# Kernel tuning notes

Measured on AMD Instinct MI355X. Metric: run time of the kernel, lower is better.

## Reference

```python
import jax, jax.numpy as jnp
import numpy as np

N_GRAPHS = 512  # number of graphs in the batch
S2S_STEPS = 3   # Set2Set processing_steps


def segment_softmax(e, seg, num_seg):
    m = jax.ops.segment_max(e, seg, num_segments=num_seg)
    ex = jnp.exp(e - m[seg])
    s = jax.ops.segment_sum(ex, seg, num_segments=num_seg)
    return ex / s[seg]


def setup_inputs() -> dict:
    key = jax.random.key(0)
    ks = jax.random.split(key, 24)
    N, E, Fin, Fe, D = 30000, 480000, 25, 14, 256
    s = 0.05
    inp = {
        "x": jax.random.normal(ks[0], (N, Fin), jnp.float32),
        "edge_attr": jax.random.normal(ks[1], (E, Fe), jnp.float32),
        # lin0
        "W0": jax.random.normal(ks[2], (Fin, D), jnp.float32) * s,
        "b0": jnp.zeros((D,), jnp.float32),
        # DMPNN edge-message MLP: [x_src || e_attr] -> D -> D
        "Wm1": jax.random.normal(ks[3], (D + Fe, D), jnp.float32) * s,
        "bm1": jnp.zeros((D,), jnp.float32),
        "Wm2": jax.random.normal(ks[4], (D, D), jnp.float32) * s,
        "bm2": jnp.zeros((D,), jnp.float32),
        # node (root) update
        "Wr": jax.random.normal(ks[5], (D, D), jnp.float32) * s,
        "br": jnp.zeros((D,), jnp.float32),
        # Set2Set LSTM: input 2D -> hidden D
        "Wih": jax.random.normal(ks[6], (2 * D, 4 * D), jnp.float32) * s,
        "Whh": jax.random.normal(ks[7], (D, 4 * D), jnp.float32) * s,
        "bl": jnp.zeros((4 * D,), jnp.float32),
        # readout MLP
        "W1": jax.random.normal(ks[8], (2 * D, D), jnp.float32) * s,
        "b1": jnp.zeros((D,), jnp.float32),
        "W2": jax.random.normal(ks[9], (D, 1), jnp.float32) * s,
        "b2": jnp.zeros((1,), jnp.float32),
        "edge_index": jax.random.randint(ks[10], (2, E), 0, N, jnp.int32),
        "batch": jnp.sort(jax.random.randint(ks[11], (N,), 0, N_GRAPHS, jnp.int32)),
    }
    return inp


def reference(x, edge_attr, W0, b0, Wm1, bm1, Wm2, bm2, Wr, br,
              Wih, Whh, bl, W1, b1, W2, b2, edge_index, batch):
    N = x.shape[0]
    # lin0 + relu
    h0 = jax.nn.relu(x @ W0 + b0)  # [N, D]
    # DMPNNLayer2: edge-conditioned message, sum-aggregate, root update (eval: no dropout)
    src, dst = edge_index[0], edge_index[1]
    m = jax.nn.relu(jnp.concatenate([h0[src], edge_attr], axis=-1) @ Wm1 + bm1)  # [E, D]
    m = m @ Wm2 + bm2
    agg = jax.ops.segment_sum(m, dst, num_segments=N)  # [N, D]
    out = jax.nn.relu(h0 @ Wr + br + agg)  # relu in top-level forward, massage_depth=1
    # Set2Set pooling (processing_steps=3)
    D = out.shape[1]
    B = N_GRAPHS
    q_star = jnp.zeros((B, 2 * D), out.dtype)
    h = jnp.zeros((B, D), out.dtype)
    c = jnp.zeros((B, D), out.dtype)
    for _ in range(S2S_STEPS):
        gates = q_star @ Wih + h @ Whh + bl  # [B, 4D]
        i, f, g, o = jnp.split(gates, 4, axis=-1)
        c = jax.nn.sigmoid(f) * c + jax.nn.sigmoid(i) * jnp.tanh(g)
        h = jax.nn.sigmoid(o) * jnp.tanh(c)
        e = jnp.sum(out * h[batch], axis=-1)              # [N]
        a = segment_softmax(e, batch, B)                  # [N]
        r = jax.ops.segment_sum(a[:, None] * out, batch, num_segments=B)  # [B, D]
        q_star = jnp.concatenate([h, r], axis=-1)
    # readout (eval: dropout identity)
    y = jax.nn.relu(q_star @ W1 + b1)
    y = y @ W2 + b2
    return y.reshape(-1)
```

## Files before the change

### kernel.cpp

```cpp
#include <hip/hip_runtime.h>

typedef unsigned short u16;
typedef unsigned char u8;
typedef unsigned int u32;
using s16x8 = __attribute__((ext_vector_type(8))) short;
using s16x4 = __attribute__((ext_vector_type(4))) short;
using f32x4 = __attribute__((ext_vector_type(4))) float;

#define DEV static __device__ __forceinline__

DEV float b2f(u16 u) { return __uint_as_float(((u32)u) << 16); }
DEV u16 f2bu(float f) {
    u32 u = __float_as_uint(f);
    u32 r = (u + 0x7FFFu + ((u >> 16) & 1u)) >> 16;
    return (u16)r;
}
DEV float sigm(float x) { return 1.0f / (1.0f + expf(-x)); }

DEV float ldv(const void* p, int i, int f32flag) {
    if (f32flag) return ((const float*)p)[i];
    return b2f(((const u16*)p)[i]);
}
DEV void stv(void* p, int i, float v, int f32flag) {
    if (f32flag) ((float*)p)[i] = v;
    else ((u16*)p)[i] = f2bu(v);
}

DEV int lower_bound(const int* b, int n, int v) {
    int lo = 0, hi = n;
    while (lo < hi) { int mid = (lo + hi) >> 1; if (b[mid] < v) lo = mid + 1; else hi = mid; }
    return lo;
}

__global__ void DMPNN_Change_678604832935_kernel(int* p) {
    if (p && threadIdx.x == 0 && blockIdx.x == 0) p[0] = 1;
}

__global__ void detect_kernel(const void* x, int* flag) {
    __shared__ int cnt[128];
    int tid = threadIdx.x;
    if (tid < 128) {
        u16 v = ((const u16*)x)[tid];
        int e = (v >> 7) & 0xFF;
        cnt[tid] = (e >= 100 && e <= 141) ? 1 : 0;
    }
    __syncthreads();
    if (tid == 0) {
        int s = 0;
        for (int i = 0; i < 128; ++i) s += cnt[i];
        flag[0] = (s < 110) ? 1 : 0;
    }
}

__global__ void fillv_kernel(void* out, const int* flag, float v) {
    int i = blockIdx.x * 256 + threadIdx.x;
    if (i < 512) stv(out, i, v, flag[0]);
}

__global__ void zero_kernel(float* p, int n) {
    int i = blockIdx.x * 256 + threadIdx.x;
    int stride = gridDim.x * 256;
    for (; i < n; i += stride) p[i] = 0.0f;
}

__global__ void zero2_kernel(float* a, int na, float* b, int nb) {
    int i = blockIdx.x * 256 + threadIdx.x;
    int stride = gridDim.x * 256;
    for (int j = i; j < na; j += stride) a[j] = 0.0f;
    for (int j = i; j < nb; j += stride) b[j] = 0.0f;
}

__global__ void hist_kernel(const int* __restrict__ eidx, u32* __restrict__ cnt) {
    int i = blockIdx.x * 256 + threadIdx.x;
    if (i < 480000) atomicAdd(&cnt[eidx[480000 + i]], 1u);
}

__global__ void scan1_kernel(const u32* __restrict__ cnt, u32* __restrict__ part) {
    __shared__ u32 s[256];
    int i = blockIdx.x * 256 + threadIdx.x;
    s[threadIdx.x] = (i < 30000) ? cnt[i] : 0u;
    __syncthreads();
    for (int st = 128; st > 0; st >>= 1) {
        if (threadIdx.x < st) s[threadIdx.x] += s[threadIdx.x + st];
        __syncthreads();
    }
    if (threadIdx.x == 0) part[blockIdx.x] = s[0];
}

__global__ void scan2_kernel(const u32* __restrict__ part, u32* __restrict__ pexcl, int nb) {
    int tid = threadIdx.x;
    u32 v = (tid < nb) ? part[tid] : 0u;
    u32 x = v;
    #pragma unroll
    for (int off = 1; off < 64; off <<= 1) {
        u32 t = __shfl_up(x, off, 64);
        if ((tid & 63) >= off) x += t;
    }
    __shared__ u32 wsum;
    if (tid == 63) wsum = x;
    __syncthreads();
    u32 add = (tid >= 64) ? wsum : 0u;
    if (tid < nb) pexcl[tid] = x + add - v;
}

__global__ void scan3_kernel(u32* __restrict__ cursor, const u32* __restrict__ pexcl) {
    __shared__ u32 s[256];
    int b = blockIdx.x, tid = threadIdx.x;
    int i = b * 256 + tid;
    u32 v = (i < 30000) ? cursor[i] : 0u;
    s[tid] = v;
    __syncthreads();
    for (int off = 1; off < 256; off <<= 1) {
        u32 t = (tid >= off) ? s[tid - off] : 0u;
        __syncthreads();
        s[tid] += t;
        __syncthreads();
    }
    u32 excl = s[tid] - v + pexcl[b];
    if (i < 30000) cursor[i] = excl;
}

__global__ void scatter_kernel(const int* __restrict__ eidx, u32* __restrict__ cursor,
                               u16* __restrict__ permLo, u8* __restrict__ permHi,
                               u16* __restrict__ srcW) {
    int i = blockIdx.x * 256 + threadIdx.x;
    if (i < 480000) {
        int d = eidx[480000 + i];
        u32 pos = atomicAdd(&cursor[d], 1u);
        permLo[pos] = (u16)(i & 0xFFFF);
        permHi[pos] = (u8)(i >> 16);
        if (srcW) srcW[pos] = (u16)eidx[i];
    }
}

__global__ void to_blocked_all(const void* Wm1, const void* Wm2, const void* Wr,
                               const void* Wih, const void* Whh, const int* flag,
                               u16* Wm1b, u16* Wm2b, u16* Wrb, u16* Wcatb) {
    const int T1 = 9 * 4 * 256 * 8;
    const int T2 = T1 + 8 * 4 * 256 * 8;
    const int T3 = T2 + 8 * 4 * 256 * 8;
    const int T4 = T3 + 24 * 4 * 1024 * 8;
    int idx = blockIdx.x * 256 + threadIdx.x;
    if (idx >= T4) return;
    int f32 = flag[0];
    if (idx < T3) {
        const void* src; u16* dst; int K; int l;
        if (idx < T1)      { src = Wm1; dst = Wm1b; K = 270; l = idx; }
        else if (idx < T2) { src = Wm2; dst = Wm2b; K = 256; l = idx - T1; }
        else               { src = Wr;  dst = Wrb;  K = 256; l = idx - T2; }
        int c = l & 7;
        int n = (l >> 3) & 255;
        int jk = l >> 11;
        int j = jk & 3, kt = jk >> 2;
        int k = kt * 32 + j * 8 + c;
        u16 v = 0;
        if (k < K) v = f2bu(ldv(src, k * 256 + n, f32));
        dst[l] = v;
    } else {
        int l = idx - T3;
        int c = l & 7;
        int n = (l >> 3) & 1023;
        int jk = l >> 13;
        int j = jk & 3, kt = jk >> 2;
        int k = kt * 32 + j * 8 + c;
        u16 v = 0;
        if (k < 512) v = f2bu(ldv(Wih, k * 1024 + n, f32));
        else if (k < 768) v = f2bu(ldv(Whh, (k - 512) * 1024 + n, f32));
        Wcatb[l] = v;
    }
}

__global__ __launch_bounds__(256) void lin0_kernel(const void* x, const void* W0,
                                                   const void* b0, const int* flag,
                                                   u16* h0b) {
    int f32 = flag[0];
    int n0 = blockIdx.x * 8, tid = threadIdx.x;
    __shared__ float xs[8][26];
    if (tid < 200) {
        int nn = tid / 25, k = tid % 25;
        xs[nn][k] = ldv(x, (n0 + nn) * 25 + k, f32);
    }
    __syncthreads();
    float wr[25];
    #pragma unroll
    for (int k = 0; k < 25; ++k) wr[k] = ldv(W0, k * 256 + tid, f32);
    float bias = ldv(b0, tid, f32);
    #pragma unroll
    for (int nn = 0; nn < 8; ++nn) {
        float a = bias;
        #pragma unroll
        for (int k = 0; k < 25; ++k) a += xs[nn][k] * wr[k];
        h0b[(n0 + nn) * 256 + tid] = f2bu(fmaxf(a, 0.0f));
    }
}

__global__ __launch_bounds__(256) void lin0q_kernel(
    const void* x, const void* W0, const void* b0, const int* flag,
    const u16* __restrict__ Wm1b, u16* __restrict__ h0b, u16* __restrict__ Qb) {
    __shared__ __attribute__((aligned(16))) u16 As[64 * 264];
    __shared__ float xs[64][26];
    const int f32 = flag[0];
    const int tid = threadIdx.x;
    const int w = tid >> 6, lane = tid & 63, quad = lane >> 4, mrow = lane & 15;
    const int row0 = blockIdx.x * 64;
    const int colb = w * 64 + mrow;

    for (int idx = tid; idx < 64 * 25; idx += 256) {
        int i = idx / 25, k = idx - i * 25;
        int row = row0 + i;
        xs[i][k] = (row < 30000) ? ldv(x, row * 25 + k, f32) : 0.0f;
    }
    float wr[25];
    #pragma unroll
    for (int k = 0; k < 25; ++k) wr[k] = ldv(W0, k * 256 + tid, f32);
    float bias = ldv(b0, tid, f32);
    __syncthreads();
    for (int i = 0; i < 64; ++i) {
        float a = bias;
        #pragma unroll
        for (int k = 0; k < 25; ++k) a += xs[i][k] * wr[k];
        u16 hb = f2bu(fmaxf(a, 0.0f));
        As[i * 264 + tid] = hb;
        int row = row0 + i;
        if (row < 30000) h0b[row * 256 + tid] = hb;
    }
    __syncthreads();

    f32x4 acc[4][4];
    f32x4 fzero = {0.f, 0.f, 0.f, 0.f};
    #pragma unroll
    for (int mi = 0; mi < 4; ++mi)
        #pragma unroll
        for (int ni = 0; ni < 4; ++ni) acc[mi][ni] = fzero;

    for (int kt = 0; kt < 8; ++kt) {
        s16x8 af[4], bf[4];
        #pragma unroll
        for (int ni = 0; ni < 4; ++ni)
            bf[ni] = *(const s16x8*)(Wm1b + (((kt * 4 + quad) * 256) + colb + ni * 16) * 8);
        #pragma unroll
        for (int mi = 0; mi < 4; ++mi)
            af[mi] = *(const s16x8*)(As + (mi * 16 + mrow) * 264 + kt * 32 + quad * 8);
        #pragma unroll
        for (int mi = 0; mi < 4; ++mi)
            #pragma unroll
            for (int ni = 0; ni < 4; ++ni)
                acc[mi][ni] = __builtin_amdgcn_mfma_f32_16x16x32_bf16(af[mi], bf[ni], acc[mi][ni], 0, 0, 0);
    }

    #pragma unroll
    for (int mi = 0; mi < 4; ++mi)
        #pragma unroll
        for (int rg = 0; rg < 4; ++rg) {
            int row = row0 + mi * 16 + quad * 4 + rg;
            if (row >= 30000) continue;
            #pragma unroll
            for (int ni = 0; ni < 4; ++ni)
                Qb[row * 256 + colb + ni * 16] = f2bu(acc[mi][ni][rg]);
        }
}

__global__ __launch_bounds__(256) void qgen_kernel(
    const u16* __restrict__ h0b, const u16* __restrict__ Wm1b,
    u16* __restrict__ Qb) {
    __shared__ __attribute__((aligned(16))) u16 As[64 * 264];
    const int tid = threadIdx.x;
    const int w = tid >> 6, lane = tid & 63, quad = lane >> 4, mrow = lane & 15;
    const int row0 = blockIdx.x * 64;
    const int colb = w * 64 + mrow;
    const int r = tid >> 2, sub = tid & 3;

    {
        int row = row0 + r;
        u16* arow = As + r * 264;
        #pragma unroll
        for (int j = 0; j < 8; ++j) {
            int c0 = sub * 64 + j * 8;
            s16x8 v = {0, 0, 0, 0, 0, 0, 0, 0};
            if (row < 30000) v = *(const s16x8*)(h0b + row * 256 + c0);
            *(s16x8*)(arow + c0) = v;
        }
    }
    __syncthreads();

    f32x4 acc[4][4];
    f32x4 fzero = {0.f, 0.f, 0.f, 0.f};
    #pragma unroll
    for (int mi = 0; mi < 4; ++mi)
        #pragma unroll
        for (int ni = 0; ni < 4; ++ni) acc[mi][ni] = fzero;

    for (int kt = 0; kt < 8; ++kt) {
        s16x8 af[4], bf[4];
        #pragma unroll
        for (int ni = 0; ni < 4; ++ni)
            bf[ni] = *(const s16x8*)(Wm1b + (((kt * 4 + quad) * 256) + colb + ni * 16) * 8);
        #pragma unroll
        for (int mi = 0; mi < 4; ++mi)
            af[mi] = *(const s16x8*)(As + (mi * 16 + mrow) * 264 + kt * 32 + quad * 8);
        #pragma unroll
        for (int mi = 0; mi < 4; ++mi)
            #pragma unroll
            for (int ni = 0; ni < 4; ++ni)
                acc[mi][ni] = __builtin_amdgcn_mfma_f32_16x16x32_bf16(af[mi], bf[ni], acc[mi][ni], 0, 0, 0);
    }

    #pragma unroll
    for (int mi = 0; mi < 4; ++mi)
        #pragma unroll
        for (int rg = 0; rg < 4; ++rg) {
            int row = row0 + mi * 16 + quad * 4 + rg;
            if (row >= 30000) continue;
            #pragma unroll
            for (int ni = 0; ni < 4; ++ni)
                Qb[row * 256 + colb + ni * 16] = f2bu(acc[mi][ni][rg]);
        }
}

#define MAXD 96
__global__ __launch_bounds__(256) void edge_mfma_node2_kernel(
    const u16* __restrict__ Qb, const void* __restrict__ eattr,
    const u16* __restrict__ srcW,
    const u16* __restrict__ permLo, const u8* __restrict__ permHi,
    const u32* __restrict__ cursor,
    const u16* __restrict__ Wm1b, const void* __restrict__ bm1,
    const int* __restrict__ flag, u16* __restrict__ aggB) {
    const int f32 = flag[0];
    const int n = blockIdx.x, tid = threadIdx.x;
    const int w = tid >> 6, lane = tid & 63, quad = lane >> 4, mrow = lane & 15;
    const int beg = (n > 0) ? (int)cursor[n - 1] : 0;
    const int end = (int)cursor[n];
    __shared__ int eids[MAXD];
    __shared__ int srcl[MAXD];
    __shared__ int sorted_s[MAXD];
    __shared__ int sortedSrc[MAXD];
    __shared__ __attribute__((aligned(16))) u16 Ae[16 * 40];

    const int colb = w * 64 + mrow;
    s16x8 bf[4];
    float bm1c[4];
    #pragma unroll
    for (int ni = 0; ni < 4; ++ni) {
        bf[ni] = *(const s16x8*)(Wm1b + (((32 + quad) * 256) + colb + ni * 16) * 8);
        bm1c[ni] = ldv(bm1, colb + ni * 16, f32);
    }

    float psum[4] = {0.f, 0.f, 0.f, 0.f};
    const f32x4 fzero = {0.f, 0.f, 0.f, 0.f};

    for (int base = beg; base < end; base += MAXD) {
        int wcnt = end - base; if (wcnt > MAXD) wcnt = MAXD;
        if (tid < wcnt) {
            int si = base + tid;
            eids[tid] = (int)permLo[si] | ((int)permHi[si] << 16);
            srcl[tid] = (int)srcW[si];
        }
        __syncthreads();
        if (tid < wcnt) {
            int key = eids[tid], r2 = 0;
            for (int j = 0; j < wcnt; ++j) r2 += (eids[j] < key);
            sorted_s[r2] = key;
            sortedSrc[r2] = srcl[tid];
        }
        __syncthreads();

        for (int cb = 0; cb < wcnt; cb += 16) {
            {
                int row = tid >> 4, c = tid & 15;
                int gi = cb + row;
                int e = (gi < wcnt) ? sorted_s[gi] : -1;
                u16 v = 0;
                if (e >= 0 && c < 14) v = f2bu(ldv(eattr, e * 14 + c, f32));
                Ae[row * 40 + c] = v;
                Ae[row * 40 + 16 + c] = 0;
            }
            __syncthreads();

            float qv[4][4];
            #pragma unroll
            for (int rg = 0; rg < 4; ++rg) {
                int gi = cb + quad * 4 + rg;
                int sidx = (gi < wcnt) ? sortedSrc[gi] : 0;
                const u16* qrow = Qb + sidx * 256;
                #pragma unroll
                for (int ni = 0; ni < 4; ++ni)
                    qv[rg][ni] = b2f(qrow[colb + ni * 16]);
            }

            s16x8 af = *(const s16x8*)(Ae + mrow * 40 + quad * 8);
            f32x4 acc[4];
            #pragma unroll
            for (int ni = 0; ni < 4; ++ni)
                acc[ni] = __builtin_amdgcn_mfma_f32_16x16x32_bf16(af, bf[ni], fzero, 0, 0, 0);

            #pragma unroll
            for (int rg = 0; rg < 4; ++rg) {
                if (cb + quad * 4 + rg < wcnt) {
                    #pragma unroll
                    for (int ni = 0; ni < 4; ++ni)
                        psum[ni] += fmaxf(acc[ni][rg] + bm1c[ni] + qv[rg][ni], 0.0f);
                }
            }
            __syncthreads();
        }
    }

    #pragma unroll
    for (int ni = 0; ni < 4; ++ni) {
        float v = psum[ni];
        v += __shfl_xor(v, 16, 64);
        v += __shfl_xor(v, 32, 64);
        psum[ni] = v;
    }
    if (quad == 0) {
        #pragma unroll
        for (int ni = 0; ni < 4; ++ni)
            aggB[n * 256 + colb + ni * 16] = f2bu(psum[ni]);
    }
}

__global__ __launch_bounds__(256) void edge_mfma_node_kernel(
    const u16* __restrict__ Qb, const void* __restrict__ eattr,
    const int* __restrict__ eidx,
    const u16* __restrict__ permLo, const u8* __restrict__ permHi,
    const u32* __restrict__ cursor,
    const u16* __restrict__ Wm1b, const void* __restrict__ bm1,
    const int* __restrict__ flag, float* __restrict__ aggP) {
    const int f32 = flag[0];
    const int n = blockIdx.x, tid = threadIdx.x;
    const int w = tid >> 6, lane = tid & 63, quad = lane >> 4, mrow = lane & 15;
    const int beg = (n > 0) ? (int)cursor[n - 1] : 0;
    const int end = (int)cursor[n];
    __shared__ int eids[MAXD];
    __shared__ int sorted_s[MAXD];
    __shared__ int srcs16[16];
    __shared__ __attribute__((aligned(16))) u16 Ae[16 * 40];

    const int colb = w * 64 + mrow;
    s16x8 bf[4];
    float bm1c[4];
    #pragma unroll
    for (int ni = 0; ni < 4; ++ni) {
        bf[ni] = *(const s16x8*)(Wm1b + (((32 + quad) * 256) + colb + ni * 16) * 8);
        bm1c[ni] = ldv(bm1, colb + ni * 16, f32);
    }

    float psum[4] = {0.f, 0.f, 0.f, 0.f};
    const f32x4 fzero = {0.f, 0.f, 0.f, 0.f};

    for (int base = beg; base < end; base += MAXD) {
        int wcnt = end - base; if (wcnt > MAXD) wcnt = MAXD;
        if (tid < wcnt) {
            int si = base + tid;
            eids[tid] = (int)permLo[si] | ((int)permHi[si] << 16);
        }
        __syncthreads();
        if (tid < wcnt) {
            int key = eids[tid], r2 = 0;
            for (int j = 0; j < wcnt; ++j) r2 += (eids[j] < key);
            sorted_s[r2] = key;
        }
        __syncthreads();

        for (int cb = 0; cb < wcnt; cb += 16) {
            {
                int row = tid >> 4, c = tid & 15;
                int gi = cb + row;
                int e = (gi < wcnt) ? sorted_s[gi] : -1;
                u16 v = 0;
                if (e >= 0 && c < 14) v = f2bu(ldv(eattr, e * 14 + c, f32));
                Ae[row * 40 + c] = v;
                Ae[row * 40 + 16 + c] = 0;
                if (c == 0) srcs16[row] = (e >= 0) ? eidx[e] : 0;
            }
            __syncthreads();

            s16x8 af = *(const s16x8*)(Ae + mrow * 40 + quad * 8);
            f32x4 acc[4];
            #pragma unroll
            for (int ni = 0; ni < 4; ++ni)
                acc[ni] = __builtin_amdgcn_mfma_f32_16x16x32_bf16(af, bf[ni], fzero, 0, 0, 0);

            #pragma unroll
            for (int rg = 0; rg < 4; ++rg) {
                int row = quad * 4 + rg;
                if (cb + row < wcnt) {
                    const u16* qrow = Qb + srcs16[row] * 256;
                    #pragma unroll
                    for (int ni = 0; ni < 4; ++ni) {
                        float q = b2f(qrow[colb + ni * 16]);
                        psum[ni] += fmaxf(acc[ni][rg] + bm1c[ni] + q, 0.0f);
                    }
                }
            }
            __syncthreads();
        }
    }

    #pragma unroll
    for (int ni = 0; ni < 4; ++ni) {
        float v = psum[ni];
        v += __shfl_xor(v, 16, 64);
        v += __shfl_xor(v, 32, 64);
        psum[ni] = v;
    }
    if (quad == 0) {
        #pragma unroll
        for (int ni = 0; ni < 4; ++ni)
            aggP[n * 256 + colb + ni * 16] = psum[ni];
    }
}

__global__ __launch_bounds__(256) void edge_sorted_kernel(
    const u16* __restrict__ h0b, const void* __restrict__ eattr,
    const int* __restrict__ eidx,
    const u16* __restrict__ permLo, const u8* __restrict__ permHi,
    const u16* __restrict__ Wm1b,
    const void* __restrict__ bm1,
    const int* __restrict__ flag, float* __restrict__ aggP) {
    __shared__ __attribute__((aligned(16))) u16 As[64 * 296];
    __shared__ int dsh[64];
    const int f32 = flag[0];
    const int tid = threadIdx.x;
    const int w = tid >> 6, lane = tid & 63, quad = lane >> 4, mrow = lane & 15;
    const int eb0 = blockIdx.x * 64;
    const int colb = w * 64 + mrow;

    if (tid < 64) {
        int sj = eb0 + tid;
        int ee = (int)permLo[sj] | ((int)permHi[sj] << 16);
        dsh[tid] = eidx[480000 + ee];
    }
    {
        int r = tid >> 2, sub = tid & 3;
        int si = eb0 + r;
        int e = (int)permLo[si] | ((int)permHi[si] << 16);
        int src = eidx[e];
        const u16* hrow = h0b + src * 256;
        u16* arow = As + r * 296;
        #pragma unroll
        for (int j = 0; j < 8; ++j) {
            int c0 = sub * 64 + j * 8;
            *(s16x8*)(arow + c0) = *(const s16x8*)(hrow + c0);
        }
        if (sub == 0) {
            for (int c = 0; c < 14; ++c) arow[256 + c] = f2bu(ldv(eattr, e * 14 + c, f32));
            for (int c = 14; c < 40; ++c) arow[256 + c] = 0;
        }
    }
    __syncthreads();

    f32x4 acc[4][4];
    f32x4 fzero = {0.f, 0.f, 0.f, 0.f};
    #pragma unroll
    for (int mi = 0; mi < 4; ++mi)
        #pragma unroll
        for (int ni = 0; ni < 4; ++ni) acc[mi][ni] = fzero;

    for (int kt = 0; kt < 9; ++kt) {
        s16x8 af[4], bf[4];
        #pragma unroll
        for (int ni = 0; ni < 4; ++ni)
            bf[ni] = *(const s16x8*)(Wm1b + (((kt * 4 + quad) * 256) + colb + ni * 16) * 8);
        #pragma unroll
        for (int mi = 0; mi < 4; ++mi)
            af[mi] = *(const s16x8*)(As + (mi * 16 + mrow) * 296 + kt * 32 + quad * 8);
        #pragma unroll
        for (int mi = 0; mi < 4; ++mi)
            #pragma unroll
            for (int ni = 0; ni < 4; ++ni)
                acc[mi][ni] = __builtin_amdgcn_mfma_f32_16x16x32_bf16(af[mi], bf[ni], acc[mi][ni], 0, 0, 0);
    }

    float bm1c[4];
    #pragma unroll
    for (int ni = 0; ni < 4; ++ni) bm1c[ni] = ldv(bm1, colb + ni * 16, f32);
    __syncthreads();
    #pragma unroll
    for (int mi = 0; mi < 4; ++mi)
        #pragma unroll
        for (int ni = 0; ni < 4; ++ni)
            #pragma unroll
            for (int rg = 0; rg < 4; ++rg) {
                int row = mi * 16 + quad * 4 + rg;
                As[row * 296 + colb + ni * 16] = f2bu(fmaxf(acc[mi][ni][rg] + bm1c[ni], 0.0f));
            }
    __syncthreads();

    {
        int c = tid;
        float s = 0.0f;
        int cur = dsh[0];
        #pragma unroll 8
        for (int rr = 0; rr < 64; ++rr) {
            int d = dsh[rr];
            if (d != cur) { atomicAdd(&aggP[cur * 256 + c], s); s = 0.0f; cur = d; }
            s += b2f(As[rr * 296 + c]);
        }
        atomicAdd(&aggP[cur * 256 + c], s);
    }
}

__global__ __launch_bounds__(256) void node_dual_kernel(
    u16* __restrict__ h0b, const u16* __restrict__ Wrb, const u16* __restrict__ Wm2b,
    const void* __restrict__ br, const void* __restrict__ bm2,
    const void* __restrict__ aggV, int agg_bf16,
    const u32* __restrict__ cursor,
    const int* __restrict__ flag) {
    __shared__ __attribute__((aligned(16))) u16 As[64 * 264];
    const int f32 = flag[0];
    const int tid = threadIdx.x;
    const int w = tid >> 6, lane = tid & 63, quad = lane >> 4, mrow = lane & 15;
    const int row0 = blockIdx.x * 64;
    const int colb = w * 64 + mrow;
    const int r = tid >> 2, sub = tid & 3;

    {
        int row = row0 + r;
        u16* arow = As + r * 264;
        #pragma unroll
        for (int j = 0; j < 8; ++j) {
            int c0 = sub * 64 + j * 8;
            s16x8 v = {0, 0, 0, 0, 0, 0, 0, 0};
            if (row < 30000) v = *(const s16x8*)(h0b + row * 256 + c0);
            *(s16x8*)(arow + c0) = v;
        }
    }
    __syncthreads();

    f32x4 acc[4][4];
    f32x4 fzero = {0.f, 0.f, 0.f, 0.f};
    #pragma unroll
    for (int mi = 0; mi < 4; ++mi)
        #pragma unroll
        for (int ni = 0; ni < 4; ++ni) acc[mi][ni] = fzero;

    for (int kt = 0; kt < 8; ++kt) {
        s16x8 af[4], bf[4];
        #pragma unroll
        for (int ni = 0; ni < 4; ++ni)
            bf[ni] = *(const s16x8*)(Wrb + (((kt * 4 + quad) * 256) + colb + ni * 16) * 8);
        #pragma unroll
        for (int mi = 0; mi < 4; ++mi)
            af[mi] = *(const s16x8*)(As + (mi * 16 + mrow) * 264 + kt * 32 + quad * 8);
        #pragma unroll
        for (int mi = 0; mi < 4; ++mi)
            #pragma unroll
            for (int ni = 0; ni < 4; ++ni)
                acc[mi][ni] = __builtin_amdgcn_mfma_f32_16x16x32_bf16(af[mi], bf[ni], acc[mi][ni], 0, 0, 0);
    }
    __syncthreads();

    {
        int row = row0 + r;
        u16* arow = As + r * 264;
        if (agg_bf16) {
            const u16* aggB = (const u16*)aggV;
            #pragma unroll
            for (int j = 0; j < 8; ++j) {
                int c0 = sub * 64 + j * 8;
                s16x8 v = {0, 0, 0, 0, 0, 0, 0, 0};
                if (row < 30000) v = *(const s16x8*)(aggB + row * 256 + c0);
                *(s16x8*)(arow + c0) = v;
            }
        } else {
            const float* aggP = (const float*)aggV;
            #pragma unroll
            for (int j = 0; j < 8; ++j) {
                int c0 = sub * 64 + j * 8;
                s16x8 pk = {0, 0, 0, 0, 0, 0, 0, 0};
                if (row < 30000) {
                    f32x4 a = *(const f32x4*)(aggP + row * 256 + c0);
                    f32x4 b = *(const f32x4*)(aggP + row * 256 + c0 + 4);
                    pk[0] = (short)f2bu(a[0]); pk[1] = (short)f2bu(a[1]);
                    pk[2] = (short)f2bu(a[2]); pk[3] = (short)f2bu(a[3]);
                    pk[4] = (short)f2bu(b[0]); pk[5] = (short)f2bu(b[1]);
                    pk[6] = (short)f2bu(b[2]); pk[7] = (short)f2bu(b[3]);
                }
                *(s16x8*)(arow + c0) = pk;
            }
        }
    }
    __syncthreads();

    for (int kt = 0; kt < 8; ++kt) {
        s16x8 af[4], bf[4];
        #pragma unroll
        for (int ni = 0; ni < 4; ++ni)
            bf[ni] = *(const s16x8*)(Wm2b + (((kt * 4 + quad) * 256) + colb + ni * 16) * 8);
        #pragma unroll
        for (int mi = 0; mi < 4; ++mi)
            af[mi] = *(const s16x8*)(As + (mi * 16 + mrow) * 264 + kt * 32 + quad * 8);
        #pragma unroll
        for (int mi = 0; mi < 4; ++mi)
            #pragma unroll
            for (int ni = 0; ni < 4; ++ni)
                acc[mi][ni] = __builtin_amdgcn_mfma_f32_16x16x32_bf16(af[mi], bf[ni], acc[mi][ni], 0, 0, 0);
    }

    #pragma unroll
    for (int mi = 0; mi < 4; ++mi)
        #pragma unroll
        for (int rg = 0; rg < 4; ++rg) {
            int row = row0 + mi * 16 + quad * 4 + rg;
            if (row >= 30000) continue;
            float dg = (float)(cursor[row] - (row > 0 ? cursor[row - 1] : 0u));
            #pragma unroll
            for (int ni = 0; ni < 4; ++ni) {
                int col = colb + ni * 16;
                float v = acc[mi][ni][rg] + ldv(br, col, f32) + dg * ldv(bm2, col, f32);
                h0b[row * 256 + col] = f2bu(fmaxf(v, 0.0f));
            }
        }
}

__global__ __launch_bounds__(256) void gates_mfma_kernel(
    const u16* __restrict__ Abuf, const u16* __restrict__ Wcatb,
    float* __restrict__ G) {
    const int tid = threadIdx.x;
    const int w = tid >> 6, lane = tid & 63, quad = lane >> 4, mrow = lane & 15;
    const int row0 = blockIdx.x * 64;
    const int col = blockIdx.y * 64 + w * 16 + mrow;

    f32x4 acc[4];
    f32x4 fzero = {0.f, 0.f, 0.f, 0.f};
    #pragma unroll
    for (int mi = 0; mi < 4; ++mi) acc[mi] = fzero;

    for (int kt = 0; kt < 24; ++kt) {
        s16x8 bfv = *(const s16x8*)(Wcatb + (((kt * 4 + quad) * 1024) + col) * 8);
        s16x8 af[4];
        #pragma unroll
        for (int mi = 0; mi < 4; ++mi)
            af[mi] = *(const s16x8*)(Abuf + (row0 + mi * 16 + mrow) * 768 + kt * 32 + quad * 8);
        #pragma unroll
        for (int mi = 0; mi < 4; ++mi)
            acc[mi] = __builtin_amdgcn_mfma_f32_16x16x32_bf16(af[mi], bfv, acc[mi], 0, 0, 0);
    }

    #pragma unroll
    for (int mi = 0; mi < 4; ++mi)
        #pragma unroll
        for (int rg = 0; rg < 4; ++rg)
            G[(row0 + mi * 16 + quad * 4 + rg) * 1024 + col] = acc[mi][rg];
}

#define GROWS 112
__global__ __launch_bounds__(256) void s2s_lstm_fused_kernel(
    const float* __restrict__ G, const void* __restrict__ bl,
    const int* __restrict__ flag, float* __restrict__ Cst, float* __restrict__ Hst,
    const u16* __restrict__ outb, const int* __restrict__ batch,
    float* __restrict__ Rst, u16* __restrict__ Abuf, float* __restrict__ ebuf) {
    __shared__ __attribute__((aligned(16))) u16 Ls[GROWS * 256];
    __shared__ __attribute__((aligned(16))) float hsh[256];
    __shared__ float esh[GROWS];
    __shared__ float red[256];
    const int b = blockIdx.x, tid = threadIdx.x;
    const int w = tid >> 6, lane = tid & 63;
    const int f32 = flag[0];

    {
        float gi = G[b * 1024 + tid]       + ldv(bl, tid, f32);
        float gf = G[b * 1024 + 256 + tid] + ldv(bl, 256 + tid, f32);
        float gg = G[b * 1024 + 512 + tid] + ldv(bl, 512 + tid, f32);
        float go = G[b * 1024 + 768 + tid] + ldv(bl, 768 + tid, f32);
        float c = Cst[b * 256 + tid];
        c = sigm(gf) * c + sigm(gi) * tanhf(gg);
        Cst[b * 256 + tid] = c;
        float h = sigm(go) * tanhf(c);
        Hst[b * 256 + tid] = h;
        u16 hb = f2bu(h);
        Abuf[b * 768 + tid] = hb;
        Abuf[b * 768 + 512 + tid] = hb;
        hsh[tid] = h;
    }
    const int n0 = lower_bound(batch, 30000, b);
    const int n1 = lower_bound(batch, 30000, b + 1);
    const int cnt = n1 - n0;
    __syncthreads();
    float r_out = 0.0f;
    if (cnt > 0 && cnt <= GROWS) {
        for (int idx = tid; idx < cnt * 32; idx += 256) {
            int i = idx >> 5, c8 = idx & 31;
            *(s16x8*)(Ls + i * 256 + c8 * 8) = *(const s16x8*)(outb + (n0 + i) * 256 + c8 * 8);
        }
        __syncthreads();
        for (int i = w; i < cnt; i += 4) {
            s16x4 ov = *(const s16x4*)(Ls + i * 256 + lane * 4);
            f32x4 hv = *(const f32x4*)(hsh + lane * 4);
            float p = b2f((u16)ov[0]) * hv[0] + b2f((u16)ov[1]) * hv[1]
                    + b2f((u16)ov[2]) * hv[2] + b2f((u16)ov[3]) * hv[3];
            #pragma unroll
            for (int off = 1; off < 64; off <<= 1) p += __shfl_xor(p, off, 64);
            if (lane == 0) esh[i] = p;
        }
        __syncthreads();
        float m = -1e30f;
        for (int i = tid; i < cnt; i += 256) m = fmaxf(m, esh[i]);
        red[tid] = m; __syncthreads();
        for (int s = 128; s > 0; s >>= 1) { if (tid < s) red[tid] = fmaxf(red[tid], red[tid + s]); __syncthreads(); }
        m = red[0]; __syncthreads();
        float sl = 0.0f;
        for (int i = tid; i < cnt; i += 256) { float pe = expf(esh[i] - m); esh[i] = pe; sl += pe; }
        red[tid] = sl; __syncthreads();
        for (int s = 128; s > 0; s >>= 1) { if (tid < s) red[tid] += red[tid + s]; __syncthreads(); }
        float ssum = red[0]; __syncthreads();
        float acc = 0.0f;
        for (int i = 0; i < cnt; ++i) acc += esh[i] * b2f(Ls[i * 256 + tid]);
        r_out = acc / ssum;
    } else if (cnt > GROWS) {
        for (int i = w; i < cnt; i += 4) {
            const u16* orow = outb + (n0 + i) * 256 + lane * 4;
            f32x4 hv = *(const f32x4*)(hsh + lane * 4);
            float p = b2f(orow[0]) * hv[0] + b2f(orow[1]) * hv[1]
                    + b2f(orow[2]) * hv[2] + b2f(orow[3]) * hv[3];
            #pragma unroll
            for (int off = 1; off < 64; off <<= 1) p += __shfl_xor(p, off, 64);
            if (lane == 0) ebuf[n0 + i] = p;
        }
        __syncthreads();
        float m = -1e30f;
        for (int n = n0 + tid; n < n1; n += 256) m = fmaxf(m, ebuf[n]);
        red[tid] = m; __syncthreads();
        for (int s = 128; s > 0; s >>= 1) { if (tid < s) red[tid] = fmaxf(red[tid], red[tid + s]); __syncthreads(); }
        m = red[0]; __syncthreads();
        float sl = 0.0f;
        for (int n = n0 + tid; n < n1; n += 256) sl += expf(ebuf[n] - m);
        red[tid] = sl; __syncthreads();
        for (int s = 128; s > 0; s >>= 1) { if (tid < s) red[tid] += red[tid + s]; __syncthreads(); }
        float ssum = red[0]; __syncthreads();
        float acc = 0.0f;
        for (int c0 = n0; c0 < n1; c0 += 256) {
            int nn = n1 - c0; if (nn > 256) nn = 256;
            __syncthreads();
            if (tid < nn) red[tid] = expf(ebuf[c0 + tid] - m);
            __syncthreads();
            for (int i = 0; i < nn; ++i) acc += red[i] * b2f(outb[(c0 + i) * 256 + tid]);
        }
        r_out = acc / ssum;
    }
    Rst[b * 256 + tid] = r_out;
    Abuf[b * 768 + 256 + tid] = f2bu(r_out);
}

__global__ __launch_bounds__(256) void readout_kernel(const float* Hst, const float* Rst,
                                                      const void* W1, const void* b1,
                                                      const void* W2, const void* b2,
                                                      const u16* nodeout, const void* aggV,
                                                      int agg_bf16,
                                                      const int* flag, void* out) {
    int f32 = flag[0];
    int b = blockIdx.x, tid = threadIdx.x;
    __shared__ float qs[512];
    __shared__ float red[256];
    qs[tid] = Hst[b * 256 + tid];
    qs[256 + tid] = Rst[b * 256 + tid];
    __syncthreads();
    float a = ldv(b1, tid, f32);
    if (f32) {
        const float* W1f = (const float*)W1;
        #pragma unroll 8
        for (int k = 0; k < 512; ++k) a += qs[k] * W1f[k * 256 + tid];
    } else {
        const u16* W1h = (const u16*)W1;
        #pragma unroll 8
        for (int k = 0; k < 512; ++k) a += qs[k] * b2f(W1h[k * 256 + tid]);
    }
    a = fmaxf(a, 0.0f) * ldv(W2, tid, f32);
    red[tid] = a; __syncthreads();
    for (int s = 128; s > 0; s >>= 1) { if (tid < s) red[tid] += red[tid + s]; __syncthreads(); }
    if (tid == 0) {
        float D = 0.0f;
        if (b == 0) {
            float s1 = 0.0f, s2 = 0.0f, s3 = 0.0f;
            for (int i = 0; i < 256; ++i) {
                s1 += fabsf(b2f(nodeout[i]));
                s2 += agg_bf16 ? fabsf(b2f(((const u16*)aggV)[i]))
                               : fabsf(((const float*)aggV)[i]);
                s3 += fabsf(Rst[i]);
            }
            if (s1 < 1e-3f) D += 100.0f;
            if (s2 < 1e-3f) D += 200.0f;
            if (s3 < 1e-6f) D += 400.0f;
        }
        stv(out, b, red[0] + ldv(b2, 0, f32) + D, f32);
    }
}

#define OFF_FLAG 0
#define OFF_HST  64
#define OFF_RST  524352
#define OFF_CST  1048640
#define OFF_PLO  64
#define OFF_PHI  960064
#define OFF_CUR  1440064
#define OFF_WREG 1572928
#define OFF_WM1B (OFF_WREG)
#define OFF_WM2B (OFF_WREG + 147456)
#define OFF_WRB  (OFF_WREG + 278528)
#define OFF_WCAT (OFF_WREG + 409600)
#define OFF_E    3670080
#define OFF_AGG  3790144
#define OFF_ABUF (OFF_AGG + 1048576)
#define OFF_G    (OFF_AGG + 4194304)
#define OFF_H0B  34510144
#define WS_NEEDED 49870144
#define OFF_Q    49870144
#define WS_FAST  (49870144 + 15360000)
#define OFF_SRC  (OFF_Q + 15360000)
#define WS_FAST2 (OFF_SRC + 960000)

extern "C" __attribute__((visibility("default")))
void kernel_launch(void* const* d_in, const int* in_sizes, int n_in,
                   void* d_out, int out_size, void* d_ws, size_t ws_size,
                   hipStream_t stream) {
    char* ws = (char*)d_ws;
    int*   flag   = (int*)(ws + OFF_FLAG);
    float* Hst    = (float*)(ws + OFF_HST);
    float* Rst    = (float*)(ws + OFF_RST);
    float* Cst    = (float*)(ws + OFF_CST);
    u16*   permLo = (u16*)(ws + OFF_PLO);
    u8*    permHi = (u8*)(ws + OFF_PHI);
    u32*   cursor = (u32*)(ws + OFF_CUR);
    u16*   Wm1b   = (u16*)(ws + OFF_WM1B);
    u16*   Wm2b   = (u16*)(ws + OFF_WM2B);
    u16*   Wrb    = (u16*)(ws + OFF_WRB);
    u16*   Wcatb  = (u16*)(ws + OFF_WCAT);
    float* ebuf   = (float*)(ws + OFF_E);
    u32*   part   = (u32*)(ws + OFF_E);
    u32*   pexcl  = (u32*)(ws + OFF_E + 512);
    float* aggP   = (float*)(ws + OFF_AGG);
    u16*   Abuf   = (u16*)(ws + OFF_ABUF);
    float* G      = (float*)(ws + OFF_G);
    u16*   h0b    = (u16*)(ws + OFF_H0B);
    u16*   Qb     = (u16*)(ws + OFF_Q);
    u16*   srcW   = (u16*)(ws + OFF_SRC);

    detect_kernel<<<1, 256, 0, stream>>>(d_in[0], flag);

    bool sizes_ok = (n_in == 19)
        && in_sizes[0] == 30000 * 25
        && in_sizes[1] == 480000 * 14
        && in_sizes[4] == 270 * 256
        && in_sizes[10] == 512 * 1024
        && in_sizes[17] == 2 * 480000
        && in_sizes[18] == 30000;
    if (!sizes_ok) { fillv_kernel<<<2, 256, 0, stream>>>(d_out, flag, 1600.0f); return; }
    if (ws_size < (size_t)WS_NEEDED) { fillv_kernel<<<2, 256, 0, stream>>>(d_out, flag, 800.0f); return; }
    const int fastlvl = (ws_size >= (size_t)WS_FAST2) ? 2
                      : (ws_size >= (size_t)WS_FAST)  ? 1 : 0;

    fillv_kernel<<<2, 256, 0, stream>>>(d_out, flag, 3.0f);
    DMPNN_Change_678604832935_kernel<<<1, 64, 0, stream>>>((int*)(ws + OFF_G));

    const void* x     = d_in[0];
    const void* eattr = d_in[1];
    const void* W0    = d_in[2];
    const void* b0    = d_in[3];
    const void* Wm1   = d_in[4];
    const void* bm1   = d_in[5];
    const void* Wm2   = d_in[6];
    const void* bm2   = d_in[7];
    const void* Wr    = d_in[8];
    const void* br    = d_in[9];
    const void* Wih   = d_in[10];
    const void* Whh   = d_in[11];
    const void* bl    = d_in[12];
    const void* W1    = d_in[13];
    const void* b1    = d_in[14];
    const void* W2    = d_in[15];
    const void* b2    = d_in[16];
    const int* eidx   = (const int*)d_in[17];
    const int* batch  = (const int*)d_in[18];

    to_blocked_all<<<3872, 256, 0, stream>>>(Wm1, Wm2, Wr, Wih, Whh, flag,
                                             Wm1b, Wm2b, Wrb, Wcatb);

    if (fastlvl >= 1) {
        lin0q_kernel<<<469, 256, 0, stream>>>(x, W0, b0, flag, Wm1b, h0b, Qb);
    } else {
        lin0_kernel<<<3750, 256, 0, stream>>>(x, W0, b0, flag, h0b);
    }

    zero_kernel<<<30, 256, 0, stream>>>((float*)cursor, 30000);
    hist_kernel<<<1875, 256, 0, stream>>>(eidx, cursor);
    scan1_kernel<<<118, 256, 0, stream>>>(cursor, part);
    scan2_kernel<<<1, 128, 0, stream>>>(part, pexcl, 118);
    scan3_kernel<<<118, 256, 0, stream>>>(cursor, pexcl);
    scatter_kernel<<<1875, 256, 0, stream>>>(eidx, cursor, permLo, permHi,
                                             (fastlvl == 2) ? srcW : (u16*)nullptr);

    int agg_bf16 = 0;
    if (fastlvl == 2) {
        agg_bf16 = 1;
        edge_mfma_node2_kernel<<<30000, 256, 0, stream>>>(Qb, eattr, srcW, permLo, permHi,
                                                          cursor, Wm1b, bm1, flag,
                                                          (u16*)aggP);
    } else if (fastlvl == 1) {
        edge_mfma_node_kernel<<<30000, 256, 0, stream>>>(Qb, eattr, eidx, permLo, permHi,
                                                         cursor, Wm1b, bm1, flag, aggP);
    } else {
        zero_kernel<<<1024, 256, 0, stream>>>(aggP, 7680000);
        edge_sorted_kernel<<<7500, 256, 0, stream>>>(h0b, eattr, eidx, permLo, permHi,
                                                     Wm1b, bm1, flag, aggP);
    }
    node_dual_kernel<<<469, 256, 0, stream>>>(h0b, Wrb, Wm2b, br, bm2,
                                              aggP, agg_bf16, cursor, flag);

    zero2_kernel<<<256, 256, 0, stream>>>(Cst, 131072, (float*)Abuf, 196608);

    for (int s = 0; s < 3; ++s) {
        gates_mfma_kernel<<<dim3(8, 16), 256, 0, stream>>>(Abuf, Wcatb, G);
        s2s_lstm_fused_kernel<<<512, 256, 0, stream>>>(G, bl, flag, Cst, Hst,
                                                       h0b, batch, Rst, Abuf, ebuf);
    }
    readout_kernel<<<512, 256, 0, stream>>>(Hst, Rst, W1, b1, W2, b2, h0b,
                                            aggP, agg_bf16, flag, d_out);
}
```

Measured before the change: 460.9 us.

## Merge init launches, fold scan2 into scan3, pre-convert edge_attr to bf16

```diff
diff --git a/kernel.cpp b/kernel.cpp
--- a/kernel.cpp
+++ b/kernel.cpp
@@ -52,6 +52,29 @@
     }
 }
 
+__global__ void init_kernel(const void* x, int* flag, void* out, int* stub) {
+    __shared__ int cnt[128];
+    __shared__ int fsh;
+    int tid = threadIdx.x;
+    if (tid < 128) {
+        u16 v = ((const u16*)x)[tid];
+        int e = (v >> 7) & 0xFF;
+        cnt[tid] = (e >= 100 && e <= 141) ? 1 : 0;
+    }
+    __syncthreads();
+    if (tid == 0) {
+        int s = 0;
+        for (int i = 0; i < 128; ++i) s += cnt[i];
+        int f = (s < 110) ? 1 : 0;
+        flag[0] = f;
+        fsh = f;
+        if (stub) stub[0] = 1;
+    }
+    __syncthreads();
+    int f32 = fsh;
+    for (int i = tid; i < 512; i += 256) stv(out, i, 3.0f, f32);
+}
+
 __global__ void fillv_kernel(void* out, const int* flag, float v) {
     int i = blockIdx.x * 256 + threadIdx.x;
     if (i < 512) stv(out, i, v, flag[0]);
@@ -87,25 +110,21 @@
     if (threadIdx.x == 0) part[blockIdx.x] = s[0];
 }
 
-__global__ void scan2_kernel(const u32* __restrict__ part, u32* __restrict__ pexcl, int nb) {
-    int tid = threadIdx.x;
-    u32 v = (tid < nb) ? part[tid] : 0u;
-    u32 x = v;
-    #pragma unroll
-    for (int off = 1; off < 64; off <<= 1) {
-        u32 t = __shfl_up(x, off, 64);
-        if ((tid & 63) >= off) x += t;
-    }
-    __shared__ u32 wsum;
-    if (tid == 63) wsum = x;
-    __syncthreads();
-    u32 add = (tid >= 64) ? wsum : 0u;
-    if (tid < nb) pexcl[tid] = x + add - v;
-}
-
-__global__ void scan3_kernel(u32* __restrict__ cursor, const u32* __restrict__ pexcl) {
+__global__ void scan3_kernel(u32* __restrict__ cursor, const u32* __restrict__ part) {
     __shared__ u32 s[256];
+    __shared__ u32 pbase;
     int b = blockIdx.x, tid = threadIdx.x;
+    {
+        u32 v = (tid < 118 && tid < b) ? part[tid] : 0u;
+        s[tid] = v;
+        __syncthreads();
+        for (int st = 128; st > 0; st >>= 1) {
+            if (tid < st) s[tid] += s[tid + st];
+            __syncthreads();
+        }
+        if (tid == 0) pbase = s[0];
+        __syncthreads();
+    }
     int i = b * 256 + tid;
     u32 v = (i < 30000) ? cursor[i] : 0u;
     s[tid] = v;
@@ -116,7 +135,7 @@
         s[tid] += t;
         __syncthreads();
     }
-    u32 excl = s[tid] - v + pexcl[b];
+    u32 excl = s[tid] - v + pbase;
     if (i < 30000) cursor[i] = excl;
 }
 
@@ -134,15 +153,24 @@
 }
 
 __global__ void to_blocked_all(const void* Wm1, const void* Wm2, const void* Wr,
-                               const void* Wih, const void* Whh, const int* flag,
-                               u16* Wm1b, u16* Wm2b, u16* Wrb, u16* Wcatb) {
+                               const void* Wih, const void* Whh,
+                               const void* eattr, const int* flag,
+                               u16* Wm1b, u16* Wm2b, u16* Wrb, u16* Wcatb,
+                               u16* eattrB) {
     const int T1 = 9 * 4 * 256 * 8;
     const int T2 = T1 + 8 * 4 * 256 * 8;
     const int T3 = T2 + 8 * 4 * 256 * 8;
     const int T4 = T3 + 24 * 4 * 1024 * 8;
+    const int T5 = T4 + 480000 * 14;
     int idx = blockIdx.x * 256 + threadIdx.x;
-    if (idx >= T4) return;
     int f32 = flag[0];
+    if (idx >= T4) {
+        if (eattrB && idx < T5) {
+            int l = idx - T4;
+            eattrB[l] = f2bu(ldv(eattr, l, f32));
+        }
+        return;
+    }
     if (idx < T3) {
         const void* src; u16* dst; int K; int l;
         if (idx < T1)      { src = Wm1; dst = Wm1b; K = 270; l = idx; }
@@ -320,6 +348,7 @@
 #define MAXD 96
 __global__ __launch_bounds__(256) void edge_mfma_node2_kernel(
     const u16* __restrict__ Qb, const void* __restrict__ eattr,
+    const u16* __restrict__ eattrB,
     const u16* __restrict__ srcW,
     const u16* __restrict__ permLo, const u8* __restrict__ permHi,
     const u32* __restrict__ cursor,
@@ -370,7 +399,8 @@
                 int gi = cb + row;
                 int e = (gi < wcnt) ? sorted_s[gi] : -1;
                 u16 v = 0;
-                if (e >= 0 && c < 14) v = f2bu(ldv(eattr, e * 14 + c, f32));
+                if (e >= 0 && c < 14)
+                    v = eattrB ? eattrB[e * 14 + c] : f2bu(ldv(eattr, e * 14 + c, f32));
                 Ae[row * 40 + c] = v;
                 Ae[row * 40 + 16 + c] = 0;
             }
@@ -909,6 +939,8 @@
 #define WS_FAST  (49870144 + 15360000)
 #define OFF_SRC  (OFF_Q + 15360000)
 #define WS_FAST2 (OFF_SRC + 960000)
+#define OFF_EATB (OFF_SRC + 960000)
+#define WS_FAST3 (OFF_EATB + 13440000)
 
 extern "C" __attribute__((visibility("default")))
 void kernel_launch(void* const* d_in, const int* in_sizes, int n_in,
@@ -928,15 +960,13 @@
     u16*   Wcatb  = (u16*)(ws + OFF_WCAT);
     float* ebuf   = (float*)(ws + OFF_E);
     u32*   part   = (u32*)(ws + OFF_E);
-    u32*   pexcl  = (u32*)(ws + OFF_E + 512);
     float* aggP   = (float*)(ws + OFF_AGG);
     u16*   Abuf   = (u16*)(ws + OFF_ABUF);
     float* G      = (float*)(ws + OFF_G);
     u16*   h0b    = (u16*)(ws + OFF_H0B);
     u16*   Qb     = (u16*)(ws + OFF_Q);
     u16*   srcW   = (u16*)(ws + OFF_SRC);
-
-    detect_kernel<<<1, 256, 0, stream>>>(d_in[0], flag);
+    u16*   eattrB = (u16*)(ws + OFF_EATB);
 
     bool sizes_ok = (n_in == 19)
         && in_sizes[0] == 30000 * 25
@@ -945,13 +975,19 @@
         && in_sizes[10] == 512 * 1024
         && in_sizes[17] == 2 * 480000
         && in_sizes[18] == 30000;
-    if (!sizes_ok) { fillv_kernel<<<2, 256, 0, stream>>>(d_out, flag, 1600.0f); return; }
-    if (ws_size < (size_t)WS_NEEDED) { fillv_kernel<<<2, 256, 0, stream>>>(d_out, flag, 800.0f); return; }
-    const int fastlvl = (ws_size >= (size_t)WS_FAST2) ? 2
+    if (!sizes_ok) {
+        detect_kernel<<<1, 256, 0, stream>>>(d_in[0], flag);
+        fillv_kernel<<<2, 256, 0, stream>>>(d_out, flag, 1600.0f);
+        return;
+    }
+    if (ws_size < (size_t)WS_NEEDED) {
+        detect_kernel<<<1, 256, 0, stream>>>(d_in[0], flag);
+        fillv_kernel<<<2, 256, 0, stream>>>(d_out, flag, 800.0f);
+        return;
+    }
+    const int fastlvl = (ws_size >= (size_t)WS_FAST3) ? 3
+                      : (ws_size >= (size_t)WS_FAST2) ? 2
                       : (ws_size >= (size_t)WS_FAST)  ? 1 : 0;
-
-    fillv_kernel<<<2, 256, 0, stream>>>(d_out, flag, 3.0f);
-    DMPNN_Change_678604832935_kernel<<<1, 64, 0, stream>>>((int*)(ws + OFF_G));
 
     const void* x     = d_in[0];
     const void* eattr = d_in[1];
@@ -973,8 +1009,15 @@
     const int* eidx   = (const int*)d_in[17];
     const int* batch  = (const int*)d_in[18];
 
-    to_blocked_all<<<3872, 256, 0, stream>>>(Wm1, Wm2, Wr, Wih, Whh, flag,
-                                             Wm1b, Wm2b, Wrb, Wcatb);
+    init_kernel<<<1, 256, 0, stream>>>(x, flag, d_out, (int*)(ws + OFF_G));
+
+    {
+        int total = (fastlvl >= 3) ? (991232 + 480000 * 14) : 991232;
+        int grid = (total + 255) / 256;
+        to_blocked_all<<<grid, 256, 0, stream>>>(Wm1, Wm2, Wr, Wih, Whh, eattr, flag,
+                                                 Wm1b, Wm2b, Wrb, Wcatb,
+                                                 (fastlvl >= 3) ? eattrB : (u16*)nullptr);
+    }
 
     if (fastlvl >= 1) {
         lin0q_kernel<<<469, 256, 0, stream>>>(x, W0, b0, flag, Wm1b, h0b, Qb);
@@ -985,17 +1028,16 @@
     zero_kernel<<<30, 256, 0, stream>>>((float*)cursor, 30000);
     hist_kernel<<<1875, 256, 0, stream>>>(eidx, cursor);
     scan1_kernel<<<118, 256, 0, stream>>>(cursor, part);
-    scan2_kernel<<<1, 128, 0, stream>>>(part, pexcl, 118);
-    scan3_kernel<<<118, 256, 0, stream>>>(cursor, pexcl);
+    scan3_kernel<<<118, 256, 0, stream>>>(cursor, part);
     scatter_kernel<<<1875, 256, 0, stream>>>(eidx, cursor, permLo, permHi,
-                                             (fastlvl == 2) ? srcW : (u16*)nullptr);
+                                             (fastlvl >= 2) ? srcW : (u16*)nullptr);
 
     int agg_bf16 = 0;
-    if (fastlvl == 2) {
+    if (fastlvl >= 2) {
         agg_bf16 = 1;
-        edge_mfma_node2_kernel<<<30000, 256, 0, stream>>>(Qb, eattr, srcW, permLo, permHi,
-                                                          cursor, Wm1b, bm1, flag,
-                                                          (u16*)aggP);
+        edge_mfma_node2_kernel<<<30000, 256, 0, stream>>>(
+            Qb, eattr, (fastlvl >= 3) ? eattrB : (u16*)nullptr,
+            srcW, permLo, permHi, cursor, Wm1b, bm1, flag, (u16*)aggP);
     } else if (fastlvl == 1) {
         edge_mfma_node_kernel<<<30000, 256, 0, stream>>>(Qb, eattr, eidx, permLo, permHi,
                                                          cursor, Wm1b, bm1, flag, aggP);
```

Result: no change. 460.0 us (-0.2%).
